# Kernel optimization log

Hardware: AMD Instinct MI355X
Metric: run time of the kernel (lower is better)

## Reference

```python
import jax, jax.numpy as jnp
import numpy as np

HIDDEN = 512
HEADS = 8
HEAD_DIM = HIDDEN // HEADS   # 64
MAN_DIM = 256                # manifold_dim = hidden_dim // 2
SCALE = HEAD_DIM ** -0.5


def _c(re, im):
    return jax.lax.complex(re, im)


def setup_inputs() -> dict:
    key = jax.random.key(0)
    ks = jax.random.split(key, 13)
    def w(k, shape, fan_in):
        return (jax.random.normal(k, shape, dtype=jnp.float32) / np.sqrt(fan_in)).astype(jnp.float32)
    B, S = 2, 2048
    return {
        "x": jax.random.normal(ks[0], (B, S, HIDDEN), dtype=jnp.float32),
        "Wq_re": w(ks[1], (HIDDEN, HIDDEN), HIDDEN), "Wq_im": w(ks[2], (HIDDEN, HIDDEN), HIDDEN),
        "Wk_re": w(ks[3], (HIDDEN, HIDDEN), HIDDEN), "Wk_im": w(ks[4], (HIDDEN, HIDDEN), HIDDEN),
        "Wv_re": w(ks[5], (HIDDEN, HIDDEN), HIDDEN), "Wv_im": w(ks[6], (HIDDEN, HIDDEN), HIDDEN),
        "Wm_re": w(ks[7], (HEAD_DIM, MAN_DIM), HEAD_DIM), "Wm_im": w(ks[8], (HEAD_DIM, MAN_DIM), HEAD_DIM),
        "Wmi_re": w(ks[9], (MAN_DIM, HEAD_DIM), MAN_DIM), "Wmi_im": w(ks[10], (MAN_DIM, HEAD_DIM), MAN_DIM),
        "Wo_re": w(ks[11], (HIDDEN, HIDDEN), HIDDEN), "Wo_im": w(ks[12], (HIDDEN, HIDDEN), HIDDEN),
    }


def reference(x, Wq_re, Wq_im, Wk_re, Wk_im, Wv_re, Wv_im,
              Wm_re, Wm_im, Wmi_re, Wmi_im, Wo_re, Wo_im):
    B, S, D = x.shape
    # quantum state preparation: cast to complex, L2-normalize along last dim
    xc = x.astype(jnp.complex64)
    norm = jnp.linalg.norm(xc, axis=-1, keepdims=True)
    xc = xc / norm

    Wq, Wk, Wv = _c(Wq_re, Wq_im), _c(Wk_re, Wk_im), _c(Wv_re, Wv_im)
    Wm, Wmi, Wo = _c(Wm_re, Wm_im), _c(Wmi_re, Wmi_im), _c(Wo_re, Wo_im)

    def heads(t):  # [B,S,D] -> [B,H,S,head_dim]
        return t.reshape(B, S, HEADS, HEAD_DIM).transpose(0, 2, 1, 3)

    q = heads(xc @ Wq)
    k = heads(xc @ Wk)
    v = heads(xc @ Wv)

    # project each head onto the manifold (complex linear)
    qm = jnp.einsum('bhsd,dm->bhsm', q, Wm)
    km = jnp.einsum('bhsd,dm->bhsm', k, Wm)
    vm = jnp.einsum('bhsd,dm->bhsm', v, Wm)

    # Hermitian inner product attention scores; softmax over real part
    scores = jnp.einsum('bhqm,bhkm->bhqk', qm, jnp.conj(km)) * SCALE
    attn = jax.nn.softmax(scores.real, axis=-1).astype(jnp.complex64)

    outm = jnp.einsum('bhqk,bhkm->bhqm', attn, vm)
    out = jnp.einsum('bhsm,md->bhsd', outm, Wmi)        # back to head_dim
    out = out.transpose(0, 2, 1, 3).reshape(B, S, D)    # merge heads
    out = out @ Wo
    # return real/imag stacked as float32 (complex64 output -> [B,S,D,2])
    return jnp.stack([out.real, out.imag], axis=-1)
```

## Files before the change

### kernel.cpp

```cpp
#include <hip/hip_runtime.h>
#include <hip/hip_bf16.h>
#include <stdint.h>


typedef __attribute__((ext_vector_type(8))) short bf16x8;
typedef __attribute__((ext_vector_type(4))) float f32x4;

#define QSCALE 0.18033688011112042f

__device__ __forceinline__ unsigned short f2b(float f) {
    union { float f; unsigned int u; } v; v.f = f;
    unsigned int r = v.u + 0x7fffu + ((v.u >> 16) & 1u);
    return (unsigned short)(r >> 16);
}

__device__ __forceinline__ float b2f(short s) {
    union { float f; unsigned int u; } v;
    v.u = ((unsigned int)(unsigned short)s) << 16;
    return v.f;
}

__device__ __forceinline__ unsigned int cvtpk(float a, float b) {
    union { __hip_bfloat162 h; unsigned int u; } v;
    v.h = __float22bfloat162_rn(make_float2(a, b));
    return v.u;
}

__device__ __forceinline__ void ld16(void* lds, const void* g) {
    __builtin_amdgcn_global_load_lds(
        (__attribute__((address_space(1))) unsigned int*)(g),
        (__attribute__((address_space(3))) unsigned int*)(lds), 16, 0, 0);
}

__global__ __launch_bounds__(256) void k_prep(
        const float* __restrict__ x, unsigned short* __restrict__ xn,
        const float* __restrict__ Wq_re, const float* __restrict__ Wq_im,
        const float* __restrict__ Wk_re, const float* __restrict__ Wk_im,
        const float* __restrict__ Wv_re, const float* __restrict__ Wv_im,
        const float* __restrict__ Wm_re, const float* __restrict__ Wm_im,
        unsigned short* __restrict__ WqkvT, unsigned short* __restrict__ Bq,
        float* __restrict__ WmT_re, float* __restrict__ WmT_im) {
    __shared__ float tile[64][65];
    if (blockIdx.x < 1024) {
        int row  = blockIdx.x * 4 + (threadIdx.x >> 6);
        int lane = threadIdx.x & 63;
        const float4* xr = (const float4*)(x + (size_t)row * 512);
        float4 a = xr[lane], b = xr[lane + 64];
        float s = a.x*a.x + a.y*a.y + a.z*a.z + a.w*a.w
                + b.x*b.x + b.y*b.y + b.z*b.z + b.w*b.w;
        #pragma unroll
        for (int m = 1; m < 64; m <<= 1) s += __shfl_xor(s, m, 64);
        float inv = 1.0f / sqrtf(s);
        ushort4 o;
        o.x = f2b(a.x*inv); o.y = f2b(a.y*inv); o.z = f2b(a.z*inv); o.w = f2b(a.w*inv);
        *(ushort4*)&xn[(size_t)row*512 + lane*4] = o;
        o.x = f2b(b.x*inv); o.y = f2b(b.y*inv); o.z = f2b(b.z*inv); o.w = f2b(b.w*inv);
        *(ushort4*)&xn[(size_t)row*512 + 256 + lane*4] = o;
        return;
    }
    int bid = blockIdx.x - 1024;
    int tx = threadIdx.x & 63, ty = threadIdx.x >> 6;
    if (bid < 256) {
        int mat = bid >> 6, tl = bid & 63;
        const float* src = (mat==0)?Wk_re:(mat==1)?Wk_im:(mat==2)?Wv_re:Wv_im;
        int r0 = (tl >> 3) * 64, c0 = (tl & 7) * 64;
        #pragma unroll
        for (int i = 0; i < 16; i++) {
            int r = ty + i*4;
            tile[r][tx] = src[(size_t)(r0 + r)*512 + c0 + tx];
        }
        __syncthreads();
        int sec = 1024 + (mat >> 1)*1024, part = mat & 1;
        #pragma unroll
        for (int i = 0; i < 16; i++) {
            int r = ty + i*4;
            int rr = c0 + r, h = rr >> 6, j = rr & 63;
            WqkvT[(size_t)(sec + h*128 + part*64 + j)*512 + r0 + tx] = f2b(tile[tx][r]);
        }
    } else if (bid < 264) {
        int mat = (bid - 256) >> 2, tl = (bid - 256) & 3;
        const float* src = mat ? Wm_im : Wm_re;
        float* dst = mat ? WmT_im : WmT_re;
        int c0 = tl * 64;
        #pragma unroll
        for (int i = 0; i < 16; i++) {
            int r = ty + i*4;
            tile[r][tx] = src[(size_t)r*256 + c0 + tx];
        }
        __syncthreads();
        #pragma unroll
        for (int i = 0; i < 16; i++) {
            int r = ty + i*4;
            dst[(size_t)(c0 + r)*64 + tx] = tile[tx][r];
        }
    } else {
        int b3 = bid - 264;
        int mat = b3 >> 6, tl = b3 & 63;
        const float* src = mat ? Wq_im : Wq_re;
        #pragma unroll
        for (int i = 0; i < 16; i++) {
            int idx = tl*4096 + i*256 + threadIdx.x;
            int k = idx >> 9, col = idx & 511;
            int h = col >> 6, d = col & 63;
            Bq[(size_t)(h*512 + k)*128 + mat*64 + d] = f2b(src[(size_t)k*512 + col]);
        }
    }
}

__global__ __launch_bounds__(256) void k_gh(const float* __restrict__ Wm_re, const float* __restrict__ Wm_im,
                                            const float* __restrict__ WmT_re, const float* __restrict__ WmT_im,
                                            const float* __restrict__ Wmi_re, const float* __restrict__ Wmi_im,
                                            float* __restrict__ GH, unsigned short* __restrict__ Aq) {
    int id = blockIdx.x * 256 + threadIdx.x;
    int mat = id >> 12;
    int a = (id >> 6) & 63, c = id & 63;
    float s = 0.f;
    if (mat < 2) {
        for (int m = 0; m < 256; m++) {
            float ar = Wm_re[a*256+m], ai = Wm_im[a*256+m];
            float br = WmT_re[m*64+c], bi = WmT_im[m*64+c];
            s += (mat == 0) ? (ar*br + ai*bi) : (ai*br - ar*bi);
        }
        float sq = s * QSCALE;
        if (mat == 0) {
            Aq[c*128 + a]           = f2b(sq);
            Aq[(64+c)*128 + 64 + a] = f2b(sq);
        } else {
            Aq[(64+c)*128 + a]      = f2b(sq);
            Aq[c*128 + 64 + a]      = f2b(-sq);
        }
    } else {
        for (int m = 0; m < 256; m++) {
            float ar = Wm_re[a*256+m], ai = Wm_im[a*256+m];
            float br = Wmi_re[m*64+c], bi = Wmi_im[m*64+c];
            s += (mat == 2) ? (ar*br - ai*bi) : (ar*bi + ai*br);
        }
        GH[mat*4096 + c*64 + a] = s;
    }
}

__global__ __launch_bounds__(256) void k_packwo(
        const float* __restrict__ Wo_re,  const float* __restrict__ Wo_im,
        const float* __restrict__ GH, unsigned short* __restrict__ Wbig) {
    int id = blockIdx.x * 256 + threadIdx.x;
    int np = id >> 10, kk = id & 1023;
    int c = np >> 1, p = np & 1;
    int h = kk >> 7, pp = (kk >> 6) & 1, d = kk & 63;
    const float* HrT = GH + 2*4096;
    const float* HiT = GH + 3*4096;
    float s = 0.f;
    if (p == pp) {
        for (int j = 0; j < 64; j++) {
            float hr = HrT[j*64+d], hi = HiT[j*64+d];
            float wr = Wo_re[(size_t)(h*64+j)*512 + c];
            float wi = Wo_im[(size_t)(h*64+j)*512 + c];
            s += hr*wr - hi*wi;
        }
    } else {
        for (int j = 0; j < 64; j++) {
            float hr = HrT[j*64+d], hi = HiT[j*64+d];
            float wr = Wo_re[(size_t)(h*64+j)*512 + c];
            float wi = Wo_im[(size_t)(h*64+j)*512 + c];
            s += hr*wi + hi*wr;
        }
        if (p == 0) s = -s;
    }
    Wbig[(size_t)np*1024 + kk] = f2b(s);
}

template<int MODE, int MT, int MW>
__global__ __launch_bounds__(256, MW) void k_gemm(
        const unsigned short* __restrict__ Ain, const unsigned short* __restrict__ Btin,
        void* __restrict__ Cout, unsigned short* __restrict__ Vt, int K) {
    __shared__ __align__(16) unsigned short Al[2][MT*32];
    __shared__ __align__(16) unsigned short Bl[2][128*32];
    const int t = threadIdx.x;
    const int wave = t >> 6, lane = t & 63, quad = lane >> 4, l16 = lane & 15;
    const int wr = wave >> 1, wc = wave & 1;

    const unsigned short* A;
    const unsigned short* Bt;
    unsigned short* Cb = nullptr;
    int m0, n0;
    if (MODE == 0) {
        if (blockIdx.y < 16) {
            A = Ain; Bt = Btin;
            m0 = blockIdx.x * 128; n0 = blockIdx.y * 128;
            Cb = (unsigned short*)Cout;
        } else {
            int idx = (blockIdx.y - 16) * 32 + blockIdx.x;
            int b = idx >> 7, mt = (idx >> 4) & 7, nt = idx & 15;
            A  = Btin + 2048*512;
            Bt = Ain + (size_t)b*2048*512;
            m0 = mt * 128; n0 = nt * 128;
            Cb = Vt + (size_t)b*1024*2048;
        }
    } else {
        A = Ain; Bt = Btin;
        m0 = blockIdx.x * MT; n0 = blockIdx.y * 128;
    }

    f32x4 acc[MT/32][4] = {};
    for (int kt = 0; kt < K; kt += 64) {
        #pragma unroll
        for (int kh = 0; kh < 2; kh++)
            #pragma unroll
            for (int i = 0; i < MT/64; i++) {
                int g = t + i*256, r = g >> 2, gr = g & 3;
                ld16(&Al[kh][g*8], &A[(size_t)(m0 + r)*K + kt + kh*32 + gr*8]);
            }
        #pragma unroll
        for (int kh = 0; kh < 2; kh++)
            #pragma unroll
            for (int i = 0; i < 2; i++) {
                int g = t + i*256, r = g >> 2, gr = g & 3;
                ld16(&Bl[kh][g*8], &Bt[(size_t)(n0 + r)*K + kt + kh*32 + gr*8]);
            }
        __syncthreads();
        #pragma unroll
        for (int kh = 0; kh < 2; kh++) {
            bf16x8 af[MT/32], bfr[4];
            #pragma unroll
            for (int rt = 0; rt < MT/32; rt++)
                af[rt] = *(const bf16x8*)&Al[kh][(wr*(MT/2) + rt*16 + l16)*32 + quad*8];
            #pragma unroll
            for (int ct = 0; ct < 4; ct++)
                bfr[ct] = *(const bf16x8*)&Bl[kh][(wc*64 + ct*16 + l16)*32 + quad*8];
            #pragma unroll
            for (int rt = 0; rt < MT/32; rt++)
                #pragma unroll
                for (int ct = 0; ct < 4; ct++)
                    acc[rt][ct] = __builtin_amdgcn_mfma_f32_16x16x32_bf16(af[rt], bfr[ct], acc[rt][ct], 0, 0, 0);
        }
        __syncthreads();
    }
    #pragma unroll
    for (int rt = 0; rt < MT/32; rt++) {
        int row = m0 + wr*(MT/2) + rt*16 + quad*4;
        #pragma unroll
        for (int ct = 0; ct < 4; ct++) {
            int col = n0 + wc*64 + ct*16 + l16;
            if (MODE == 0) {
                unsigned int u01 = cvtpk(acc[rt][ct][0], acc[rt][ct][1]);
                unsigned int u23 = cvtpk(acc[rt][ct][2], acc[rt][ct][3]);
                Cb[(size_t)(row+0)*2048 + col] = (unsigned short)(u01);
                Cb[(size_t)(row+1)*2048 + col] = (unsigned short)(u01 >> 16);
                Cb[(size_t)(row+2)*2048 + col] = (unsigned short)(u23);
                Cb[(size_t)(row+3)*2048 + col] = (unsigned short)(u23 >> 16);
            } else if (MODE == 2) {
                unsigned short* Cq = (unsigned short*)Cout;
                int h = col >> 9, k = col & 511;
                unsigned int u01 = cvtpk(acc[rt][ct][0], acc[rt][ct][1]);
                unsigned int u23 = cvtpk(acc[rt][ct][2], acc[rt][ct][3]);
                Cq[(size_t)(h*128 + row + 0)*512 + k] = (unsigned short)(u01);
                Cq[(size_t)(h*128 + row + 1)*512 + k] = (unsigned short)(u01 >> 16);
                Cq[(size_t)(h*128 + row + 2)*512 + k] = (unsigned short)(u23);
                Cq[(size_t)(h*128 + row + 3)*512 + k] = (unsigned short)(u23 >> 16);
            } else {
                float* C = (float*)Cout;
                #pragma unroll
                for (int r = 0; r < 4; r++)
                    C[(size_t)(row + r)*1024 + col] = acc[rt][ct][r];
            }
        }
    }
}

__global__ __launch_bounds__(256, 2) void k_attn(
        const unsigned short* __restrict__ QK,
        const unsigned short* __restrict__ Vt,
        unsigned short* __restrict__ Opart,
        float* __restrict__ Lpart) {
    __shared__ __align__(16) unsigned short Kl[2][8192];
    __shared__ __align__(16) unsigned short Vl[2][8192];
    __shared__ __align__(16) unsigned short Pl[4608];

    const int t = threadIdx.x, w = t >> 6, lane = t & 63, quad = lane >> 4, l16 = lane & 15;
    const int quadx = quad ^ ((l16 >> 2) & 3);
    const int bh = blockIdx.x, b = bh >> 3, h = bh & 7;
    const int qb = blockIdx.y & 15, half = blockIdx.y >> 4;
    const int tok0 = b*2048 + qb*128;

    bf16x8 qf[2][4];
    #pragma unroll
    for (int rt = 0; rt < 2; rt++)
        #pragma unroll
        for (int ks = 0; ks < 4; ks++)
            qf[rt][ks] = *(const bf16x8*)&QK[(size_t)(tok0 + w*32 + rt*16 + l16)*2048 + h*128 + ks*32 + quad*8];

    const int grs = (t & 3) ^ ((t >> 4) & 3);
    const unsigned short* kp = QK + (size_t)(b*2048 + half*1024 + (t >> 2))*2048 + 1024 + h*128 + grs*8;
    const unsigned short* vp = Vt + (size_t)(b*1024 + h*128 + (t >> 2))*2048 + half*1024 + grs*8;

    f32x4 Oacc[2][8] = {};
    float ls[2][4] = {};

    #pragma unroll
    for (int i = 0; i < 4; i++) ld16(&Kl[0][(i*256 + t)*8], kp + i*32);
    #pragma unroll
    for (int i = 0; i < 4; i++) ld16(&Vl[0][(i*256 + t)*8], vp + (i & 1)*131072 + (i >> 1)*32);
    __syncthreads();

    for (int it = 0; it < 16; it++) {
        const int cur = it & 1;
        if (it < 15) {
            int kt2 = (it + 1) * 64;
            #pragma unroll
            for (int i = 0; i < 4; i++) ld16(&Kl[cur^1][(i*256 + t)*8], kp + (size_t)kt2*2048 + i*32);
            #pragma unroll
            for (int i = 0; i < 4; i++) ld16(&Vl[cur^1][(i*256 + t)*8], vp + kt2 + (i & 1)*131072 + (i >> 1)*32);
        }

        f32x4 S[2][4] = {};
        #pragma unroll
        for (int ks = 0; ks < 4; ks++) {
            #pragma unroll
            for (int ct = 0; ct < 4; ct++) {
                bf16x8 kf = *(const bf16x8*)&Kl[cur][ks*2048 + (ct*16 + l16)*32 + quadx*8];
                #pragma unroll
                for (int rt = 0; rt < 2; rt++)
                    S[rt][ct] = __builtin_amdgcn_mfma_f32_16x16x32_bf16(qf[rt][ks], kf, S[rt][ct], 0, 0, 0);
            }
        }
        #pragma unroll
        for (int ks2 = 0; ks2 < 2; ks2++) {
            #pragma unroll
            for (int rt = 0; rt < 2; rt++) {
                #pragma unroll
                for (int ct2 = 0; ct2 < 2; ct2++) {
                    int ct = ks2*2 + ct2;
                    float p0 = exp2f(S[rt][ct][0]), p1 = exp2f(S[rt][ct][1]);
                    float p2 = exp2f(S[rt][ct][2]), p3 = exp2f(S[rt][ct][3]);
                    ls[rt][0] += p0; ls[rt][1] += p1; ls[rt][2] += p2; ls[rt][3] += p3;
                    int q = w*32 + rt*16 + quad*4;
                    int base = ct2*16 + l16;
                    unsigned int u01 = cvtpk(p0, p1);
                    unsigned int u23 = cvtpk(p2, p3);
                    Pl[base + (q+0)*36] = (unsigned short)(u01);
                    Pl[base + (q+1)*36] = (unsigned short)(u01 >> 16);
                    Pl[base + (q+2)*36] = (unsigned short)(u23);
                    Pl[base + (q+3)*36] = (unsigned short)(u23 >> 16);
                }
            }
            bf16x8 pf[2];
            #pragma unroll
            for (int rt = 0; rt < 2; rt++)
                pf[rt] = *(const bf16x8*)&Pl[(w*32 + rt*16 + l16)*36 + quad*8];
            #pragma unroll
            for (int dt = 0; dt < 8; dt++) {
                bf16x8 vf = *(const bf16x8*)&Vl[cur][ks2*4096 + (dt*16 + l16)*32 + quadx*8];
                #pragma unroll
                for (int rt = 0; rt < 2; rt++)
                    Oacc[rt][dt] = __builtin_amdgcn_mfma_f32_16x16x32_bf16(pf[rt], vf, Oacc[rt][dt], 0, 0, 0);
            }
        }
        __syncthreads();
    }

    #pragma unroll
    for (int rt = 0; rt < 2; rt++)
        #pragma unroll
        for (int r = 0; r < 4; r++) {
            float s = ls[rt][r];
            #pragma unroll
            for (int m = 1; m < 16; m <<= 1) s += __shfl_xor(s, m, 64);
            ls[rt][r] = s;
        }
    unsigned short* Op = Opart + (size_t)half*4096*1024;
    float* Lp = Lpart + (size_t)half*32768;
    #pragma unroll
    for (int rt = 0; rt < 2; rt++) {
        int q = w*32 + rt*16 + quad*4;
        int tok = tok0 + q;
        float inv[4];
        #pragma unroll
        for (int r = 0; r < 4; r++) inv[r] = 1.0f / ls[rt][r];
        if (l16 == 0) {
            #pragma unroll
            for (int r = 0; r < 4; r++) Lp[(size_t)(tok + r)*8 + h] = ls[rt][r];
        }
        #pragma unroll
        for (int dt = 0; dt < 8; dt++) {
            int col = h*128 + dt*16 + l16;
            #pragma unroll
            for (int r = 0; r < 4; r++)
                Op[(size_t)(tok + r)*1024 + col] = f2b(Oacc[rt][dt][r] * inv[r]);
        }
    }
}

__global__ __launch_bounds__(256) void k_merge(const unsigned short* __restrict__ Opart,
                                               const float* __restrict__ Lpart,
                                               unsigned short* __restrict__ O) {
    int slot = blockIdx.x * 256 + threadIdx.x;
    int tok = slot >> 7, colg = slot & 127, h = colg >> 4;
    float l0 = Lpart[(size_t)tok*8 + h];
    float l1 = Lpart[32768 + (size_t)tok*8 + h];
    float inv = 1.0f / (l0 + l1);
    float w0 = l0*inv, w1 = l1*inv;
    size_t off = (size_t)tok*1024 + colg*8;
    bf16x8 a0 = *(const bf16x8*)&Opart[off];
    bf16x8 a1 = *(const bf16x8*)&Opart[4194304 + off];
    float o[8];
    #pragma unroll
    for (int j = 0; j < 8; j++)
        o[j] = w0*b2f(a0[j]) + w1*b2f(a1[j]);
    uint4 uo;
    uo.x = cvtpk(o[0], o[1]); uo.y = cvtpk(o[2], o[3]);
    uo.z = cvtpk(o[4], o[5]); uo.w = cvtpk(o[6], o[7]);
    *(uint4*)&O[off] = uo;
}

extern "C" void kernel_launch(void* const* d_in, const int* in_sizes, int n_in,
                              void* d_out, int out_size, void* d_ws, size_t ws_size,
                              hipStream_t stream) {
    (void)in_sizes; (void)n_in; (void)out_size; (void)ws_size;
    const float* x      = (const float*)d_in[0];
    const float* Wq_re  = (const float*)d_in[1];
    const float* Wq_im  = (const float*)d_in[2];
    const float* Wk_re  = (const float*)d_in[3];
    const float* Wk_im  = (const float*)d_in[4];
    const float* Wv_re  = (const float*)d_in[5];
    const float* Wv_im  = (const float*)d_in[6];
    const float* Wm_re  = (const float*)d_in[7];
    const float* Wm_im  = (const float*)d_in[8];
    const float* Wmi_re = (const float*)d_in[9];
    const float* Wmi_im = (const float*)d_in[10];
    const float* Wo_re  = (const float*)d_in[11];
    const float* Wo_im  = (const float*)d_in[12];

    char* ws = (char*)d_ws;
    unsigned short* xn    = (unsigned short*)(ws);
    unsigned short* WqkvT = (unsigned short*)(ws + (4u << 20));
    unsigned short* Wbig  = (unsigned short*)(ws + (7u << 20));
    float*          GH    = (float*)         (ws + (9u << 20));
    float*          WmT_re= (float*)         (ws + (9u << 20) + (64u << 10));
    float*          WmT_im= (float*)         (ws + (9u << 20) + (128u << 10));
    unsigned short* Aq    = (unsigned short*)(ws + (9u << 20) + (192u << 10));
    unsigned short* QK    = (unsigned short*)(ws + (10u << 20));
    unsigned short* Bq    = (unsigned short*)(ws + (10u << 20));
    unsigned short* Vt    = (unsigned short*)(ws + (26u << 20));
    unsigned short* Obuf  = (unsigned short*)(ws + (34u << 20));
    unsigned short* Opart = (unsigned short*)(ws + (42u << 20));
    float*          Lpart = (float*)         (ws + (74u << 20));

    k_prep         <<<dim3(1416), dim3(256), 0, stream>>>(
        x, xn, Wq_re, Wq_im, Wk_re, Wk_im, Wv_re, Wv_im, Wm_re, Wm_im,
        WqkvT, Bq, WmT_re, WmT_im);
    k_gh           <<<dim3(64),   dim3(256), 0, stream>>>(
        Wm_re, Wm_im, WmT_re, WmT_im, Wmi_re, Wmi_im, GH, Aq);
    k_gemm<2,128,2><<<dim3(1, 32),  dim3(256), 0, stream>>>(Aq, Bq, (void*)WqkvT, nullptr, 128);
    k_packwo       <<<dim3(4096), dim3(256), 0, stream>>>(Wo_re, Wo_im, GH, Wbig);
    k_gemm<0,128,3><<<dim3(32, 24), dim3(256), 0, stream>>>(xn, WqkvT, (void*)QK, Vt, 512);
    k_attn         <<<dim3(16, 32), dim3(256), 0, stream>>>(QK, Vt, Opart, Lpart);
    k_merge        <<<dim3(2048), dim3(256), 0, stream>>>(Opart, Lpart, Obuf);
    k_gemm<1,64,2> <<<dim3(64, 8),  dim3(256), 0, stream>>>(Obuf, Wbig, d_out, nullptr, 1024);
}
```

Baseline: 239.8 us.

## Split attention keys four ways, keep P in registers via permlane swaps

The attention kernel now splits the key range into four chunks instead of two, doubling the grid, and uses 32-key tiles, which halves the K/V LDS buffers. It also computes S transposed (K as the A operand) and rebuilds the P operand for the PV MFMA in registers with permlane32/16 swaps, removing the LDS round-trip for P. Occupancy is raised to 3 blocks per CU. The merge kernel now combines four partial outputs, which adds more Opart traffic, and each block has less work to amortise its Q loads.

```diff
diff --git a/kernel.cpp b/kernel.cpp
--- a/kernel.cpp
+++ b/kernel.cpp
@@ -30,6 +30,24 @@
     __builtin_amdgcn_global_load_lds(
         (__attribute__((address_space(1))) unsigned int*)(g),
         (__attribute__((address_space(3))) unsigned int*)(lds), 16, 0, 0);
+}
+
+__device__ __forceinline__ void plswap32(unsigned int& a, unsigned int& b) {
+#if __has_builtin(__builtin_amdgcn_permlane32_swap)
+    auto r = __builtin_amdgcn_permlane32_swap(a, b, false, false);
+    a = r[0]; b = r[1];
+#else
+    asm("s_nop 0\n\tv_permlane32_swap_b32 %0, %1" : "+v"(a), "+v"(b));
+#endif
+}
+
+__device__ __forceinline__ void plswap16(unsigned int& a, unsigned int& b) {
+#if __has_builtin(__builtin_amdgcn_permlane16_swap)
+    auto r = __builtin_amdgcn_permlane16_swap(a, b, false, false);
+    a = r[0]; b = r[1];
+#else
+    asm("s_nop 0\n\tv_permlane16_swap_b32 %0, %1" : "+v"(a), "+v"(b));
+#endif
 }
 
 __global__ __launch_bounds__(256) void k_prep(
@@ -266,19 +284,18 @@
     }
 }
 
-__global__ __launch_bounds__(256, 2) void k_attn(
+__global__ __launch_bounds__(256, 3) void k_attn(
         const unsigned short* __restrict__ QK,
         const unsigned short* __restrict__ Vt,
         unsigned short* __restrict__ Opart,
         float* __restrict__ Lpart) {
-    __shared__ __align__(16) unsigned short Kl[2][8192];
-    __shared__ __align__(16) unsigned short Vl[2][8192];
-    __shared__ __align__(16) unsigned short Pl[4608];
+    __shared__ __align__(16) unsigned short Kl[2][4096];
+    __shared__ __align__(16) unsigned short Vl[2][4096];
 
     const int t = threadIdx.x, w = t >> 6, lane = t & 63, quad = lane >> 4, l16 = lane & 15;
-    const int quadx = quad ^ ((l16 >> 2) & 3);
+    const int qxr = quad ^ ((l16 >> 2) & 3);
     const int bh = blockIdx.x, b = bh >> 3, h = bh & 7;
-    const int qb = blockIdx.y & 15, half = blockIdx.y >> 4;
+    const int qb = blockIdx.y & 15, q4 = blockIdx.y >> 4;
     const int tok0 = b*2048 + qb*128;
 
     bf16x8 qf[2][4];
@@ -288,103 +305,91 @@
         for (int ks = 0; ks < 4; ks++)
             qf[rt][ks] = *(const bf16x8*)&QK[(size_t)(tok0 + w*32 + rt*16 + l16)*2048 + h*128 + ks*32 + quad*8];
 
-    const int grs = (t & 3) ^ ((t >> 4) & 3);
-    const unsigned short* kp = QK + (size_t)(b*2048 + half*1024 + (t >> 2))*2048 + 1024 + h*128 + grs*8;
-    const unsigned short* vp = Vt + (size_t)(b*1024 + h*128 + (t >> 2))*2048 + half*1024 + grs*8;
+    const int kr = (t >> 2) & 31;
+    const int kqo = (t & 3) ^ ((kr >> 2) & 3);
+    const unsigned short* kp = QK + (size_t)(b*2048 + q4*512 + kr)*2048 + 1024 + h*128 + (t >> 7)*32 + kqo*8;
+    const int vd = t >> 2;
+    const int vqo = (t & 3) ^ ((vd >> 2) & 3);
+    const unsigned short* vp = Vt + (size_t)(b*1024 + h*128 + vd)*2048 + q4*512 + vqo*8;
 
     f32x4 Oacc[2][8] = {};
-    float ls[2][4] = {};
-
-    #pragma unroll
-    for (int i = 0; i < 4; i++) ld16(&Kl[0][(i*256 + t)*8], kp + i*32);
-    #pragma unroll
-    for (int i = 0; i < 4; i++) ld16(&Vl[0][(i*256 + t)*8], vp + (i & 1)*131072 + (i >> 1)*32);
+    float ls[2] = {};
+
+    ld16(&Kl[0][t*8], kp);
+    ld16(&Kl[0][(t+256)*8], kp + 64);
+    ld16(&Vl[0][t*8], vp);
+    ld16(&Vl[0][(t+256)*8], vp + 131072);
     __syncthreads();
 
     for (int it = 0; it < 16; it++) {
         const int cur = it & 1;
         if (it < 15) {
-            int kt2 = (it + 1) * 64;
-            #pragma unroll
-            for (int i = 0; i < 4; i++) ld16(&Kl[cur^1][(i*256 + t)*8], kp + (size_t)kt2*2048 + i*32);
-            #pragma unroll
-            for (int i = 0; i < 4; i++) ld16(&Vl[cur^1][(i*256 + t)*8], vp + kt2 + (i & 1)*131072 + (i >> 1)*32);
-        }
-
-        f32x4 S[2][4] = {};
+            const unsigned short* kp2 = kp + (size_t)(it + 1)*65536;
+            const unsigned short* vp2 = vp + (it + 1)*32;
+            ld16(&Kl[cur^1][t*8], kp2);
+            ld16(&Kl[cur^1][(t+256)*8], kp2 + 64);
+            ld16(&Vl[cur^1][t*8], vp2);
+            ld16(&Vl[cur^1][(t+256)*8], vp2 + 131072);
+        }
+
+        f32x4 S[2][2] = {};
         #pragma unroll
         for (int ks = 0; ks < 4; ks++) {
-            #pragma unroll
-            for (int ct = 0; ct < 4; ct++) {
-                bf16x8 kf = *(const bf16x8*)&Kl[cur][ks*2048 + (ct*16 + l16)*32 + quadx*8];
-                #pragma unroll
-                for (int rt = 0; rt < 2; rt++)
-                    S[rt][ct] = __builtin_amdgcn_mfma_f32_16x16x32_bf16(qf[rt][ks], kf, S[rt][ct], 0, 0, 0);
+            bf16x8 kf0 = *(const bf16x8*)&Kl[cur][ks*1024 + l16*32 + qxr*8];
+            bf16x8 kf1 = *(const bf16x8*)&Kl[cur][ks*1024 + (16 + l16)*32 + qxr*8];
+            #pragma unroll
+            for (int rt = 0; rt < 2; rt++) {
+                S[rt][0] = __builtin_amdgcn_mfma_f32_16x16x32_bf16(kf0, qf[rt][ks], S[rt][0], 0, 0, 0);
+                S[rt][1] = __builtin_amdgcn_mfma_f32_16x16x32_bf16(kf1, qf[rt][ks], S[rt][1], 0, 0, 0);
             }
         }
-        #pragma unroll
-        for (int ks2 = 0; ks2 < 2; ks2++) {
-            #pragma unroll
-            for (int rt = 0; rt < 2; rt++) {
-                #pragma unroll
-                for (int ct2 = 0; ct2 < 2; ct2++) {
-                    int ct = ks2*2 + ct2;
-                    float p0 = exp2f(S[rt][ct][0]), p1 = exp2f(S[rt][ct][1]);
-                    float p2 = exp2f(S[rt][ct][2]), p3 = exp2f(S[rt][ct][3]);
-                    ls[rt][0] += p0; ls[rt][1] += p1; ls[rt][2] += p2; ls[rt][3] += p3;
-                    int q = w*32 + rt*16 + quad*4;
-                    int base = ct2*16 + l16;
-                    unsigned int u01 = cvtpk(p0, p1);
-                    unsigned int u23 = cvtpk(p2, p3);
-                    Pl[base + (q+0)*36] = (unsigned short)(u01);
-                    Pl[base + (q+1)*36] = (unsigned short)(u01 >> 16);
-                    Pl[base + (q+2)*36] = (unsigned short)(u23);
-                    Pl[base + (q+3)*36] = (unsigned short)(u23 >> 16);
-                }
-            }
-            bf16x8 pf[2];
+
+        bf16x8 pf[2];
+        #pragma unroll
+        for (int rt = 0; rt < 2; rt++) {
+            float p0 = exp2f(S[rt][0][0]), p1 = exp2f(S[rt][0][1]);
+            float p2 = exp2f(S[rt][0][2]), p3 = exp2f(S[rt][0][3]);
+            float p4 = exp2f(S[rt][1][0]), p5 = exp2f(S[rt][1][1]);
+            float p6 = exp2f(S[rt][1][2]), p7 = exp2f(S[rt][1][3]);
+            ls[rt] += ((p0 + p1) + (p2 + p3)) + ((p4 + p5) + (p6 + p7));
+            unsigned int a0 = cvtpk(p0, p1), c0 = cvtpk(p2, p3);
+            unsigned int a1 = cvtpk(p4, p5), c1 = cvtpk(p6, p7);
+            plswap32(a0, a1); plswap16(a0, a1);
+            plswap32(c0, c1); plswap16(c0, c1);
+            union { unsigned int u[4]; bf16x8 v; } pk;
+            pk.u[0] = a0; pk.u[1] = c0; pk.u[2] = a1; pk.u[3] = c1;
+            pf[rt] = pk.v;
+        }
+
+        #pragma unroll
+        for (int dt = 0; dt < 8; dt++) {
+            bf16x8 vf = *(const bf16x8*)&Vl[cur][(dt*16 + l16)*32 + qxr*8];
             #pragma unroll
             for (int rt = 0; rt < 2; rt++)
-                pf[rt] = *(const bf16x8*)&Pl[(w*32 + rt*16 + l16)*36 + quad*8];
-            #pragma unroll
-            for (int dt = 0; dt < 8; dt++) {
-                bf16x8 vf = *(const bf16x8*)&Vl[cur][ks2*4096 + (dt*16 + l16)*32 + quadx*8];
-                #pragma unroll
-                for (int rt = 0; rt < 2; rt++)
-                    Oacc[rt][dt] = __builtin_amdgcn_mfma_f32_16x16x32_bf16(pf[rt], vf, Oacc[rt][dt], 0, 0, 0);
-            }
+                Oacc[rt][dt] = __builtin_amdgcn_mfma_f32_16x16x32_bf16(pf[rt], vf, Oacc[rt][dt], 0, 0, 0);
         }
         __syncthreads();
     }
 
-    #pragma unroll
-    for (int rt = 0; rt < 2; rt++)
-        #pragma unroll
-        for (int r = 0; r < 4; r++) {
-            float s = ls[rt][r];
-            #pragma unroll
-            for (int m = 1; m < 16; m <<= 1) s += __shfl_xor(s, m, 64);
-            ls[rt][r] = s;
-        }
-    unsigned short* Op = Opart + (size_t)half*4096*1024;
-    float* Lp = Lpart + (size_t)half*32768;
+    unsigned short* Op = Opart + (size_t)q4*4194304;
+    float* Lp = Lpart + (size_t)q4*32768;
     #pragma unroll
     for (int rt = 0; rt < 2; rt++) {
-        int q = w*32 + rt*16 + quad*4;
-        int tok = tok0 + q;
+        float lt = ls[rt];
+        lt += __shfl_xor(lt, 16, 64);
+        lt += __shfl_xor(lt, 32, 64);
+        if (lane < 16)
+            Lp[(size_t)(tok0 + w*32 + rt*16 + l16)*8 + h] = lt;
         float inv[4];
         #pragma unroll
-        for (int r = 0; r < 4; r++) inv[r] = 1.0f / ls[rt][r];
-        if (l16 == 0) {
-            #pragma unroll
-            for (int r = 0; r < 4; r++) Lp[(size_t)(tok + r)*8 + h] = ls[rt][r];
-        }
+        for (int r = 0; r < 4; r++)
+            inv[r] = 1.0f / __shfl(lt, quad*4 + r, 64);
         #pragma unroll
         for (int dt = 0; dt < 8; dt++) {
             int col = h*128 + dt*16 + l16;
             #pragma unroll
             for (int r = 0; r < 4; r++)
-                Op[(size_t)(tok + r)*1024 + col] = f2b(Oacc[rt][dt][r] * inv[r]);
+                Op[(size_t)(tok0 + w*32 + rt*16 + quad*4 + r)*1024 + col] = f2b(Oacc[rt][dt][r] * inv[r]);
         }
     }
 }
@@ -395,16 +400,20 @@
     int slot = blockIdx.x * 256 + threadIdx.x;
     int tok = slot >> 7, colg = slot & 127, h = colg >> 4;
     float l0 = Lpart[(size_t)tok*8 + h];
-    float l1 = Lpart[32768 + (size_t)tok*8 + h];
-    float inv = 1.0f / (l0 + l1);
-    float w0 = l0*inv, w1 = l1*inv;
+    float l1 = Lpart[32768  + (size_t)tok*8 + h];
+    float l2 = Lpart[65536  + (size_t)tok*8 + h];
+    float l3 = Lpart[98304  + (size_t)tok*8 + h];
+    float inv = 1.0f / (l0 + l1 + l2 + l3);
+    float w0 = l0*inv, w1 = l1*inv, w2 = l2*inv, w3 = l3*inv;
     size_t off = (size_t)tok*1024 + colg*8;
     bf16x8 a0 = *(const bf16x8*)&Opart[off];
-    bf16x8 a1 = *(const bf16x8*)&Opart[4194304 + off];
+    bf16x8 a1 = *(const bf16x8*)&Opart[4194304  + off];
+    bf16x8 a2 = *(const bf16x8*)&Opart[8388608  + off];
+    bf16x8 a3 = *(const bf16x8*)&Opart[12582912 + off];
     float o[8];
     #pragma unroll
     for (int j = 0; j < 8; j++)
-        o[j] = w0*b2f(a0[j]) + w1*b2f(a1[j]);
+        o[j] = w0*b2f(a0[j]) + w1*b2f(a1[j]) + w2*b2f(a2[j]) + w3*b2f(a3[j]);
     uint4 uo;
     uo.x = cvtpk(o[0], o[1]); uo.y = cvtpk(o[2], o[3]);
     uo.z = cvtpk(o[4], o[5]); uo.w = cvtpk(o[6], o[7]);
@@ -452,7 +461,7 @@
     k_gemm<2,128,2><<<dim3(1, 32),  dim3(256), 0, stream>>>(Aq, Bq, (void*)WqkvT, nullptr, 128);
     k_packwo       <<<dim3(4096), dim3(256), 0, stream>>>(Wo_re, Wo_im, GH, Wbig);
     k_gemm<0,128,3><<<dim3(32, 24), dim3(256), 0, stream>>>(xn, WqkvT, (void*)QK, Vt, 512);
-    k_attn         <<<dim3(16, 32), dim3(256), 0, stream>>>(QK, Vt, Opart, Lpart);
+    k_attn         <<<dim3(16, 64), dim3(256), 0, stream>>>(QK, Vt, Opart, Lpart);
     k_merge        <<<dim3(2048), dim3(256), 0, stream>>>(Opart, Lpart, Obuf);
     k_gemm<1,64,2> <<<dim3(64, 8),  dim3(256), 0, stream>>>(Obuf, Wbig, d_out, nullptr, 1024);
 }
```

Measured after the change: 239.3 us. No clear change (-0.2%).
